# Optimization experiments

Hardware: AMD Instinct MI355X
Metric: run time of the kernel (lower is better)

Reference implementation:

```python
import jax, jax.numpy as jnp
import numpy as np

I = 256  # input size
H = 256  # hidden size
B = 128
S = 1024
EPS = 1e-5


def setup_inputs() -> dict:
    key = jax.random.key(0)
    ks = jax.random.split(key, 8)
    bound = 1.0 / np.sqrt(H)
    x = jax.random.normal(ks[0], (B, S, I), dtype=jnp.float32)
    mask = jax.random.randint(ks[1], (B, S), 0, 2) == 1
    W_ih = jax.random.uniform(ks[2], (4 * H, I), jnp.float32, -bound, bound)
    W_hh = jax.random.uniform(ks[3], (4 * H, H), jnp.float32, -bound, bound)
    b_ih = jax.random.uniform(ks[4], (4 * H,), jnp.float32, -bound, bound)
    b_hh = jax.random.uniform(ks[5], (4 * H,), jnp.float32, -bound, bound)
    gamma = jnp.ones((H,), jnp.float32)
    beta = jnp.zeros((H,), jnp.float32)
    return {"x": x, "mask": mask, "W_ih": W_ih, "W_hh": W_hh,
            "b_ih": b_ih, "b_hh": b_hh, "gamma": gamma, "beta": beta}


def _layernorm(h, gamma, beta):
    mu = jnp.mean(h, axis=-1, keepdims=True)
    var = jnp.var(h, axis=-1, keepdims=True)
    return (h - mu) * jax.lax.rsqrt(var + EPS) * gamma + beta


def reference(x, mask, W_ih, W_hh, b_ih, b_hh, gamma, beta):
    b = x.shape[0]
    h0 = jnp.zeros((b, H), x.dtype)
    c0 = jnp.zeros((b, H), x.dtype)
    out0 = jnp.zeros((b, H), x.dtype)

    def step(carry, inp):
        h, c, out = carry
        x_t, m_t = inp  # (B,I), (B,)
        hn = _layernorm(h, gamma, beta)
        gates = x_t @ W_ih.T + b_ih + hn @ W_hh.T + b_hh  # (B,4H)
        i_g, f_g, g_g, o_g = jnp.split(gates, 4, axis=-1)
        c = jax.nn.sigmoid(f_g) * c + jax.nn.sigmoid(i_g) * jnp.tanh(g_g)
        h = jax.nn.sigmoid(o_g) * jnp.tanh(c)
        # output[~mask] = h[~mask]; where mask is True the old output is kept
        out = jnp.where(m_t[:, None], out, h)
        return (h, c, out), None

    xs = (jnp.swapaxes(x, 0, 1), jnp.swapaxes(mask, 0, 1))  # (S,B,I), (S,B)
    (h, c, out), _ = jax.lax.scan(step, (h0, c0, out0), xs)
    return out
```

## Files before the change

kernel.cpp:

```cpp
#include <hip/hip_runtime.h>
#include <hip/hip_bf16.h>
#include <stdint.h>


#define Bb 128
#define Ss 1024
#define Ii 256
#define Hh 256
#define G4v 1024
#define EPSF 1e-5f

typedef __bf16 bf16;
typedef __attribute__((ext_vector_type(8))) __bf16 bf16x8;
typedef __attribute__((ext_vector_type(4))) __bf16 bf16x4;
typedef __attribute__((ext_vector_type(4))) float f32x4;
typedef unsigned int u32;
typedef unsigned long long u64;

static __device__ __forceinline__ f32x4 mfma16(bf16x8 a, bf16x8 b, f32x4 c) {
  return __builtin_amdgcn_mfma_f32_16x16x32_bf16(a, b, c, 0, 0, 0);
}
static __device__ __forceinline__ float sigm(float x) { return 1.0f / (1.0f + __expf(-x)); }
static __device__ __forceinline__ float tanhf_(float x) {
  float e = __expf(-2.0f * fabsf(x));
  float t = (1.0f - e) / (1.0f + e);
  return x < 0.0f ? -t : t;
}
static __device__ __forceinline__ bf16 bfu(unsigned short u) {
  return __builtin_bit_cast(bf16, u);
}
static __device__ __forceinline__ unsigned short ubf(bf16 b) {
  return __builtin_bit_cast(unsigned short, b);
}

__global__ void k_conv_wih(const float* __restrict__ W, bf16* __restrict__ hi,
                           bf16* __restrict__ lo) {
  int i = (blockIdx.x * 256 + threadIdx.x) * 4;
  f32x4 v = *(const f32x4*)(W + i);
  bf16x4 h_, l_;
#pragma unroll
  for (int j = 0; j < 4; ++j) {
    bf16 hh = (bf16)v[j];
    h_[j] = hh;
    l_[j] = (bf16)(v[j] - (float)hh);
  }
  *(bf16x4*)(hi + i) = h_;
  *(bf16x4*)(lo + i) = l_;
}

__global__ void k_prep_whh(const float* __restrict__ W, const float* __restrict__ gamma,
                           bf16* __restrict__ Whi, bf16* __restrict__ Wlo) {
  int tid = blockIdx.x * 256 + threadIdx.x;
  int lane = tid & 63;
  int fk = tid >> 6;
  int ntg = fk >> 3, kt = fk & 7;
  int g = ntg * 16 + (lane & 15);
  int k = kt * 32 + ((lane >> 4) << 3);
  bf16x8 rh, rl;
#pragma unroll
  for (int j = 0; j < 8; ++j) {
    float wv = W[g * Hh + k + j] * gamma[k + j];
    bf16 hh = (bf16)wv;
    rh[j] = hh;
    rl[j] = (bf16)(wv - (float)hh);
  }
  *(bf16x8*)(Whi + (size_t)tid * 8) = rh;
  *(bf16x8*)(Wlo + (size_t)tid * 8) = rl;
}

__global__ void k_prep_rd(const float* __restrict__ W, const float* __restrict__ gamma,
                          const float* __restrict__ beta, const float* __restrict__ bih,
                          const float* __restrict__ bhh, float* __restrict__ RD) {
  int g = blockIdx.x * 256 + threadIdx.x;
  float r = 0.f, d = 0.f;
  for (int k = 0; k < Hh; ++k) {
    float w = W[g * Hh + k];
    r += w * gamma[k];
    d += w * beta[k];
  }
  RD[2 * g] = r;
  RD[2 * g + 1] = d + bih[g] + bhh[g];
}

__global__ __launch_bounds__(256, 2) void k_gemm(const float* __restrict__ x,
                                                 const bf16* __restrict__ Whi,
                                                 const bf16* __restrict__ Wlo,
                                                 float* __restrict__ xw,
                                                 int t0, int Tc, int ntb) {
  __shared__ bf16 Bs[2][128 * 128];
  int bid = blockIdx.x;
  int b = bid & 127;
  int r2 = bid >> 7;
  int tb = r2 % ntb;
  int gt = r2 / ntb;
  int g0 = gt * 128;
  int tid = threadIdx.x, w = tid >> 6, lane = tid & 63;
  int li = lane & 15, lg = lane >> 4;
  char* BsB = (char*)Bs;
  int tbase = tb * 128 + 32 * w;
  f32x4 acc[2][8];
#pragma unroll
  for (int mt = 0; mt < 2; ++mt)
#pragma unroll
    for (int nt = 0; nt < 8; ++nt) acc[mt][nt] = (f32x4){0.f, 0.f, 0.f, 0.f};

  for (int kp = 0; kp < 2; ++kp) {
#pragma unroll
    for (int it = 0; it < 8; ++it) {
      int p = it * 4096 + tid * 16;
      int row = p >> 8, colb = p & 255;
      size_t goff = (size_t)(g0 + row) * 512 + kp * 256 + colb;
      int dst = row * 256 + (colb ^ ((row & 7) << 4));
      *(bf16x8*)(BsB + dst) = *(const bf16x8*)((const char*)Whi + goff);
      *(bf16x8*)(BsB + 32768 + dst) = *(const bf16x8*)((const char*)Wlo + goff);
    }
    __syncthreads();
#pragma unroll
    for (int kt = 0; kt < 4; ++kt) {
      int kl = kt * 32 + lg * 8;
      int kgl = kp * 128 + kl;
      bf16x8 ah[2], al[2];
#pragma unroll
      for (int mt = 0; mt < 2; ++mt) {
        int t = t0 + tbase + 16 * mt + li;
        const float* xp = x + ((size_t)b * Ss + t) * Ii + kgl;
        f32x4 f0 = *(const f32x4*)xp;
        f32x4 f1 = *(const f32x4*)(xp + 4);
        bf16x8 hv, lv;
#pragma unroll
        for (int j = 0; j < 4; ++j) {
          bf16 h0 = (bf16)f0[j];
          hv[j] = h0;
          lv[j] = (bf16)(f0[j] - (float)h0);
          bf16 h1 = (bf16)f1[j];
          hv[4 + j] = h1;
          lv[4 + j] = (bf16)(f1[j] - (float)h1);
        }
        ah[mt] = hv;
        al[mt] = lv;
      }
#pragma unroll
      for (int nt = 0; nt < 8; ++nt) {
        int grow = nt * 16 + li;
        int off = grow * 256 + ((kl * 2) ^ ((grow & 7) << 4));
        bf16x8 bh = *(const bf16x8*)(BsB + off);
        bf16x8 bl = *(const bf16x8*)(BsB + 32768 + off);
#pragma unroll
        for (int mt = 0; mt < 2; ++mt) {
          acc[mt][nt] = mfma16(ah[mt], bh, acc[mt][nt]);
          acc[mt][nt] = mfma16(ah[mt], bl, acc[mt][nt]);
          acc[mt][nt] = mfma16(al[mt], bh, acc[mt][nt]);
        }
      }
    }
    __syncthreads();
  }
#pragma unroll
  for (int mt = 0; mt < 2; ++mt)
#pragma unroll
    for (int nt = 0; nt < 8; ++nt)
#pragma unroll
      for (int r = 0; r < 4; ++r) {
        int tl = tbase + 16 * mt + lg * 4 + r;
        int g = g0 + nt * 16 + li;
        xw[((size_t)b * Tc + tl) * G4v + g] = acc[mt][nt][r];
      }
}

__global__ __launch_bounds__(256, 1) void k_recur(
    const bf16* __restrict__ Whi_f, const bf16* __restrict__ Wlo_f,
    const float* __restrict__ xw, const int* __restrict__ mask,
    const float* __restrict__ RD, float* __restrict__ st_h, float* __restrict__ st_c,
    float* __restrict__ st_o, u64* pub, float* __restrict__ out,
    int t0, int Tc, int first, int last) {
  __shared__ bf16 hb[2][16 * 256];
  __shared__ float murs[2][16][2];
  __shared__ float2 spw[4][16];
  __shared__ float spart[16][16][2];
  int bid = blockIdx.x;
  int grp = bid & 7, q = bid >> 3;
  int tid = threadIdx.x, w = tid >> 6, lane = tid & 63;
  int li = lane & 15, lg = lane >> 4;
  int b0 = grp * 16;
  int jloc = (q * 4 + w) * 16 + li;
  char* hbB = (char*)hb;

  bf16x8 wph[4][8], wpl[4][8];
#pragma unroll
  for (int c = 0; c < 4; ++c)
#pragma unroll
    for (int kt = 0; kt < 8; ++kt) {
      int ntg = c * 16 + q * 4 + w;
      size_t off = ((size_t)(ntg * 8 + kt) * 64 + lane) * 8;
      wph[c][kt] = *(const bf16x8*)(Whi_f + off);
      wpl[c][kt] = *(const bf16x8*)(Wlo_f + off);
      asm volatile("" : "+a"(wph[c][kt]), "+a"(wpl[c][kt]));
    }
  float Rr[4], Dd[4];
#pragma unroll
  for (int c = 0; c < 4; ++c) {
    int g = c * 256 + jloc;
    Rr[c] = RD[2 * g];
    Dd[c] = RD[2 * g + 1];
  }

  float cst[4], ost[4];
  if (first) {
#pragma unroll
    for (int i = 0; i < 16; ++i) {
      hb[0][tid * 16 + i] = (bf16)0.0f;
      hb[1][tid * 16 + i] = (bf16)0.0f;
    }
#pragma unroll
    for (int r = 0; r < 4; ++r) { cst[r] = 0.f; ost[r] = 0.f; }
    if (tid < 16) { murs[0][tid][0] = 0.f; murs[0][tid][1] = rsqrtf(EPSF); }
  } else {
    int row = tid >> 4, cs = tid & 15, jseg = cs * 16;
    float s = 0.f, ss = 0.f;
#pragma unroll
    for (int i = 0; i < 16; ++i) {
      float v = st_h[(size_t)(b0 + row) * Hh + jseg + i];
      s += v;
      ss += v * v;
      bf16 hh = (bf16)v;
      int boff = row * 512 + (((jseg + i) * 2) ^ ((row & 7) << 4));
      *(bf16*)(hbB + boff) = hh;
      *(bf16*)(hbB + 8192 + boff) = (bf16)(v - (float)hh);
    }
    spart[row][cs][0] = s;
    spart[row][cs][1] = ss;
#pragma unroll
    for (int r = 0; r < 4; ++r) {
      int m = lg * 4 + r;
      cst[r] = st_c[(size_t)(b0 + m) * Hh + jloc];
      ost[r] = st_o[(size_t)(b0 + m) * Hh + jloc];
    }
    __syncthreads();
    if (tid < 16) {
      float s2 = 0.f, ss2 = 0.f;
#pragma unroll
      for (int i = 0; i < 16; ++i) { s2 += spart[tid][i][0]; ss2 += spart[tid][i][1]; }
      float mu = s2 * (1.f / 256.f);
      float var = ss2 * (1.f / 256.f) - mu * mu;
      float rs = rsqrtf(var + EPSF);
      murs[0][tid][0] = mu * rs;
      murs[0][tid][1] = rs;
    }
  }
  __syncthreads();

  float xwv[4][4];
  int mk[4];
#pragma unroll
  for (int c = 0; c < 4; ++c)
#pragma unroll
    for (int r = 0; r < 4; ++r)
      xwv[c][r] = xw[((size_t)(b0 + lg * 4 + r) * Tc + 0) * G4v + c * 256 + jloc];
#pragma unroll
  for (int r = 0; r < 4; ++r) mk[r] = mask[(size_t)(b0 + lg * 4 + r) * Ss + t0];

  int grow = tid >> 4, gcg = tid & 15;

  for (int tl = 0; tl < Tc; ++tl) {
    int tg = t0 + tl;
    int slot = (tg + 1) & 1;
    u32 want = (u32)(tg + 1);

    f32x4 acc[4];
#pragma unroll
    for (int c = 0; c < 4; ++c) acc[c] = (f32x4){0.f, 0.f, 0.f, 0.f};
#pragma unroll
    for (int kt = 0; kt < 8; ++kt) {
      int aoff = li * 512 + (((kt * 32 + lg * 8) * 2) ^ ((li & 7) << 4));
      bf16x8 ah = *(const bf16x8*)(hbB + aoff);
      bf16x8 al = *(const bf16x8*)(hbB + 8192 + aoff);
#pragma unroll
      for (int c = 0; c < 4; ++c) {
        acc[c] = mfma16(ah, wph[c][kt], acc[c]);
        acc[c] = mfma16(ah, wpl[c][kt], acc[c]);
        acc[c] = mfma16(al, wph[c][kt], acc[c]);
      }
    }
    float mrs[4], rsv[4];
#pragma unroll
    for (int r = 0; r < 4; ++r) {
      int m = lg * 4 + r;
      mrs[r] = murs[tl & 1][m][0];
      rsv[r] = murs[tl & 1][m][1];
    }
    __syncthreads();

    float hnew[4];
#pragma unroll
    for (int r = 0; r < 4; ++r) {
      float i_ = acc[0][r] * rsv[r] - mrs[r] * Rr[0] + Dd[0] + xwv[0][r];
      float f_ = acc[1][r] * rsv[r] - mrs[r] * Rr[1] + Dd[1] + xwv[1][r];
      float g_ = acc[2][r] * rsv[r] - mrs[r] * Rr[2] + Dd[2] + xwv[2][r];
      float o_ = acc[3][r] * rsv[r] - mrs[r] * Rr[3] + Dd[3] + xwv[3][r];
      float cn = sigm(f_) * cst[r] + sigm(i_) * tanhf_(g_);
      float hn = sigm(o_) * tanhf_(cn);
      cst[r] = cn;
      ost[r] = mk[r] ? ost[r] : hn;
      hnew[r] = hn;
    }
    u64* ph = pub + (size_t)(slot * 32 + bid) * 1024;
#pragma unroll
    for (int r = 0; r < 4; ++r) {
      int m = lg * 4 + r;
      float hn = hnew[r];
      bf16 hh = (bf16)hn;
      bf16 hl = (bf16)(hn - (float)hh);
      int boff = m * 512 + ((jloc * 2) ^ ((m & 7) << 4));
      *(bf16*)(hbB + boff) = hh;
      *(bf16*)(hbB + 8192 + boff) = hl;
      u64 pv = ((u64)want << 32) | ((u32)ubf(hh) << 16) | (u32)ubf(hl);
      __hip_atomic_store(&ph[m * 64 + (w * 16 + li)], pv, __ATOMIC_RELAXED,
                         __HIP_MEMORY_SCOPE_AGENT);
    }
    {
      float sr[4], qr[4];
#pragma unroll
      for (int r = 0; r < 4; ++r) { sr[r] = hnew[r]; qr[r] = hnew[r] * hnew[r]; }
#pragma unroll
      for (int msk = 1; msk < 16; msk <<= 1)
#pragma unroll
        for (int r = 0; r < 4; ++r) {
          sr[r] += __shfl_xor(sr[r], msk);
          qr[r] += __shfl_xor(qr[r], msk);
        }
      if (li == 0)
#pragma unroll
        for (int r = 0; r < 4; ++r) spw[w][lg * 4 + r] = make_float2(sr[r], qr[r]);
    }
    if (tl == Tc - 1) {
#pragma unroll
      for (int r = 0; r < 4; ++r) {
        int m = lg * 4 + r;
        st_h[(size_t)(b0 + m) * Hh + jloc] = hnew[r];
        st_c[(size_t)(b0 + m) * Hh + jloc] = cst[r];
        st_o[(size_t)(b0 + m) * Hh + jloc] = ost[r];
      }
      if (last) {
#pragma unroll
        for (int r = 0; r < 4; ++r) out[(size_t)(b0 + lg * 4 + r) * Hh + jloc] = ost[r];
      }
    }
    {
      int tln = (tl + 1 < Tc) ? tl + 1 : Tc - 1;
#pragma unroll
      for (int c = 0; c < 4; ++c)
#pragma unroll
        for (int r = 0; r < 4; ++r)
          xwv[c][r] = xw[((size_t)(b0 + lg * 4 + r) * Tc + tln) * G4v + c * 256 + jloc];
#pragma unroll
      for (int r = 0; r < 4; ++r) mk[r] = mask[(size_t)(b0 + lg * 4 + r) * Ss + t0 + tln];
    }

    u64 gv[3][4];
    const u64* srcs[3];
#pragma unroll
    for (int pi = 0; pi < 3; ++pi) {
      int qq = (q + 1 + pi) & 3;
      int pbid = qq * 8 + grp;
      srcs[pi] = pub + (size_t)(slot * 32 + pbid) * 1024 + grow * 64 + gcg * 4;
#pragma unroll
      for (int e = 0; e < 4; ++e)
        gv[pi][e] = __hip_atomic_load(&srcs[pi][e], __ATOMIC_RELAXED,
                                      __HIP_MEMORY_SCOPE_AGENT);
    }
    {
      int cnt = 0;
      bool ok = false;
      while (!ok) {
        ok = true;
#pragma unroll
        for (int pi = 0; pi < 3; ++pi)
#pragma unroll
          for (int e = 0; e < 4; ++e)
            if ((u32)(gv[pi][e] >> 32) != want) {
              ok = false;
              gv[pi][e] = __hip_atomic_load(&srcs[pi][e], __ATOMIC_RELAXED,
                                            __HIP_MEMORY_SCOPE_AGENT);
            }
        if (++cnt > (1 << 22)) break;
      }
    }
    float su = 0.f, qu = 0.f;
#pragma unroll
    for (int pi = 0; pi < 3; ++pi) {
      int qq = (q + 1 + pi) & 3;
      int j0 = qq * 64 + gcg * 4;
      int boff = grow * 512 + ((j0 * 2) ^ ((grow & 7) << 4));
      bf16x4 h4, l4;
#pragma unroll
      for (int e = 0; e < 4; ++e) {
        u32 d = (u32)gv[pi][e];
        bf16 hh = bfu((unsigned short)(d >> 16));
        bf16 hl = bfu((unsigned short)(d & 0xffffu));
        h4[e] = hh;
        l4[e] = hl;
        float f = (float)hh + (float)hl;
        su += f;
        qu += f * f;
      }
      *(bf16x4*)(hbB + boff) = h4;
      *(bf16x4*)(hbB + 8192 + boff) = l4;
    }
#pragma unroll
    for (int msk = 1; msk < 16; msk <<= 1) {
      su += __shfl_xor(su, msk);
      qu += __shfl_xor(qu, msk);
    }
    __syncthreads();
    if (li == 0) {
      float s = su + spw[0][grow].x + spw[1][grow].x + spw[2][grow].x + spw[3][grow].x;
      float ss2 = qu + spw[0][grow].y + spw[1][grow].y + spw[2][grow].y + spw[3][grow].y;
      float mu = s * (1.f / 256.f);
      float var = ss2 * (1.f / 256.f) - mu * mu;
      float rs = rsqrtf(var + EPSF);
      murs[(tl + 1) & 1][grow][0] = mu * rs;
      murs[(tl + 1) & 1][grow][1] = rs;
    }
  }
}

extern "C" void kernel_launch(void* const* d_in, const int* in_sizes, int n_in,
                              void* d_out, int out_size, void* d_ws, size_t ws_size,
                              hipStream_t stream) {
  (void)in_sizes; (void)n_in; (void)out_size;
  const float* x = (const float*)d_in[0];
  const int* mask = (const int*)d_in[1];
  const float* Wih = (const float*)d_in[2];
  const float* Whh = (const float*)d_in[3];
  const float* bih = (const float*)d_in[4];
  const float* bhh = (const float*)d_in[5];
  const float* gamma = (const float*)d_in[6];
  const float* beta = (const float*)d_in[7];
  float* outp = (float*)d_out;
  char* ws = (char*)d_ws;

  const size_t extra = 4 * (512u << 10) + (8u << 10) + 3 * (128u << 10) +
                       (512u << 10) + (64u << 10);
  int Tc = 128;
  if (ws_size >= (size_t)1024 * 524288 + extra) Tc = 1024;
  else if (ws_size >= (size_t)512 * 524288 + extra) Tc = 512;
  else if (ws_size >= (size_t)256 * 524288 + extra) Tc = 256;

  size_t o = 0;
  auto take = [&](size_t bytes) { size_t r = o; o += (bytes + 255) & ~(size_t)255; return r; };
  size_t xw_off = take((size_t)Bb * Tc * G4v * 4);
  size_t wihh_off = take(512u << 10);
  size_t wihl_off = take(512u << 10);
  size_t whhh_off = take(512u << 10);
  size_t whhl_off = take(512u << 10);
  size_t rd_off = take(8u << 10);
  size_t sth_off = take(128u << 10);
  size_t stc_off = take(128u << 10);
  size_t sto_off = take(128u << 10);
  size_t pub_off = take(512u << 10);

  bf16* wihh = (bf16*)(ws + wihh_off);
  bf16* wihl = (bf16*)(ws + wihl_off);
  bf16* whhh = (bf16*)(ws + whhh_off);
  bf16* whhl = (bf16*)(ws + whhl_off);
  float* rd = (float*)(ws + rd_off);
  float* xwp = (float*)(ws + xw_off);
  float* sth = (float*)(ws + sth_off);
  float* stc = (float*)(ws + stc_off);
  float* sto = (float*)(ws + sto_off);
  u64* pubh = (u64*)(ws + pub_off);

  hipMemsetAsync(pubh, 0, 512u << 10, stream);
  k_conv_wih<<<dim3(256), dim3(256), 0, stream>>>(Wih, wihh, wihl);
  k_prep_whh<<<dim3(128), dim3(256), 0, stream>>>(Whh, gamma, whhh, whhl);
  k_prep_rd<<<dim3(4), dim3(256), 0, stream>>>(Whh, gamma, beta, bih, bhh, rd);

  int nchunk = Ss / Tc;
  int ntb = Tc / 128;
  for (int ci = 0; ci < nchunk; ++ci) {
    int t0 = ci * Tc;
    k_gemm<<<dim3(8 * ntb * 128), dim3(256), 0, stream>>>(x, wihh, wihl, xwp, t0, Tc, ntb);
    k_recur<<<dim3(32), dim3(256), 0, stream>>>(whhh, whhl, xwp, mask, rd, sth, stc, sto,
                                                pubh, outp, t0, Tc,
                                                ci == 0 ? 1 : 0, ci == nchunk - 1 ? 1 : 0);
  }
}
```

Measured before the change: 4.769 ms.

## Switch recurrent GEMM to fp16 split-hidden with single fp16 weight, hoist peer loads

The recurrent step now stores W_hh as a single fp16 matrix instead of bf16 hi/lo pairs. It keeps h as an fp16 hi/lo split, so each step issues 2 MFMAs per tile instead of 3, into two independent accumulators. It also issues the atomic loads of peer blocks' published hidden values earlier, before the state/output bookkeeping, so their latency overlaps that work, and it simplifies the spin-wait check. This cuts MFMA count and register pressure on the serial critical path. The cost is lower weight precision (fp16 without a lo term) and possible fp16 range issues.

```diff
diff --git a/kernel.cpp b/kernel.cpp
--- a/kernel.cpp
+++ b/kernel.cpp
@@ -11,14 +11,20 @@
 #define EPSF 1e-5f
 
 typedef __bf16 bf16;
+typedef _Float16 f16;
 typedef __attribute__((ext_vector_type(8))) __bf16 bf16x8;
 typedef __attribute__((ext_vector_type(4))) __bf16 bf16x4;
+typedef __attribute__((ext_vector_type(8))) _Float16 f16x8;
+typedef __attribute__((ext_vector_type(4))) _Float16 f16x4;
 typedef __attribute__((ext_vector_type(4))) float f32x4;
 typedef unsigned int u32;
 typedef unsigned long long u64;
 
-static __device__ __forceinline__ f32x4 mfma16(bf16x8 a, bf16x8 b, f32x4 c) {
+static __device__ __forceinline__ f32x4 mfma16b(bf16x8 a, bf16x8 b, f32x4 c) {
   return __builtin_amdgcn_mfma_f32_16x16x32_bf16(a, b, c, 0, 0, 0);
+}
+static __device__ __forceinline__ f32x4 mfma16h(f16x8 a, f16x8 b, f32x4 c) {
+  return __builtin_amdgcn_mfma_f32_16x16x32_f16(a, b, c, 0, 0, 0);
 }
 static __device__ __forceinline__ float sigm(float x) { return 1.0f / (1.0f + __expf(-x)); }
 static __device__ __forceinline__ float tanhf_(float x) {
@@ -26,11 +32,11 @@
   float t = (1.0f - e) / (1.0f + e);
   return x < 0.0f ? -t : t;
 }
-static __device__ __forceinline__ bf16 bfu(unsigned short u) {
-  return __builtin_bit_cast(bf16, u);
-}
-static __device__ __forceinline__ unsigned short ubf(bf16 b) {
-  return __builtin_bit_cast(unsigned short, b);
+static __device__ __forceinline__ unsigned short ush(f16 h) {
+  return __builtin_bit_cast(unsigned short, h);
+}
+static __device__ __forceinline__ f16 hus(unsigned short u) {
+  return __builtin_bit_cast(f16, u);
 }
 
 __global__ void k_conv_wih(const float* __restrict__ W, bf16* __restrict__ hi,
@@ -49,23 +55,17 @@
 }
 
 __global__ void k_prep_whh(const float* __restrict__ W, const float* __restrict__ gamma,
-                           bf16* __restrict__ Whi, bf16* __restrict__ Wlo) {
+                           f16* __restrict__ Wf) {
   int tid = blockIdx.x * 256 + threadIdx.x;
   int lane = tid & 63;
   int fk = tid >> 6;
   int ntg = fk >> 3, kt = fk & 7;
   int g = ntg * 16 + (lane & 15);
   int k = kt * 32 + ((lane >> 4) << 3);
-  bf16x8 rh, rl;
-#pragma unroll
-  for (int j = 0; j < 8; ++j) {
-    float wv = W[g * Hh + k + j] * gamma[k + j];
-    bf16 hh = (bf16)wv;
-    rh[j] = hh;
-    rl[j] = (bf16)(wv - (float)hh);
-  }
-  *(bf16x8*)(Whi + (size_t)tid * 8) = rh;
-  *(bf16x8*)(Wlo + (size_t)tid * 8) = rl;
+  f16x8 r;
+#pragma unroll
+  for (int j = 0; j < 8; ++j) r[j] = (f16)(W[g * Hh + k + j] * gamma[k + j]);
+  *(f16x8*)(Wf + (size_t)tid * 8) = r;
 }
 
 __global__ void k_prep_rd(const float* __restrict__ W, const float* __restrict__ gamma,
@@ -147,9 +147,9 @@
         bf16x8 bl = *(const bf16x8*)(BsB + 32768 + off);
 #pragma unroll
         for (int mt = 0; mt < 2; ++mt) {
-          acc[mt][nt] = mfma16(ah[mt], bh, acc[mt][nt]);
-          acc[mt][nt] = mfma16(ah[mt], bl, acc[mt][nt]);
-          acc[mt][nt] = mfma16(al[mt], bh, acc[mt][nt]);
+          acc[mt][nt] = mfma16b(ah[mt], bh, acc[mt][nt]);
+          acc[mt][nt] = mfma16b(ah[mt], bl, acc[mt][nt]);
+          acc[mt][nt] = mfma16b(al[mt], bh, acc[mt][nt]);
         }
       }
     }
@@ -168,12 +168,11 @@
 }
 
 __global__ __launch_bounds__(256, 1) void k_recur(
-    const bf16* __restrict__ Whi_f, const bf16* __restrict__ Wlo_f,
-    const float* __restrict__ xw, const int* __restrict__ mask,
-    const float* __restrict__ RD, float* __restrict__ st_h, float* __restrict__ st_c,
-    float* __restrict__ st_o, u64* pub, float* __restrict__ out,
-    int t0, int Tc, int first, int last) {
-  __shared__ bf16 hb[2][16 * 256];
+    const f16* __restrict__ Wf, const float* __restrict__ xw,
+    const int* __restrict__ mask, const float* __restrict__ RD,
+    float* __restrict__ st_h, float* __restrict__ st_c, float* __restrict__ st_o,
+    u64* pub, float* __restrict__ out, int t0, int Tc, int first, int last) {
+  __shared__ f16 hb[2][16 * 256];
   __shared__ float murs[2][16][2];
   __shared__ float2 spw[4][16];
   __shared__ float spart[16][16][2];
@@ -185,16 +184,14 @@
   int jloc = (q * 4 + w) * 16 + li;
   char* hbB = (char*)hb;
 
-  bf16x8 wph[4][8], wpl[4][8];
+  f16x8 wp[4][8];
 #pragma unroll
   for (int c = 0; c < 4; ++c)
 #pragma unroll
     for (int kt = 0; kt < 8; ++kt) {
       int ntg = c * 16 + q * 4 + w;
-      size_t off = ((size_t)(ntg * 8 + kt) * 64 + lane) * 8;
-      wph[c][kt] = *(const bf16x8*)(Whi_f + off);
-      wpl[c][kt] = *(const bf16x8*)(Wlo_f + off);
-      asm volatile("" : "+a"(wph[c][kt]), "+a"(wpl[c][kt]));
+      wp[c][kt] = *(const f16x8*)(Wf + ((size_t)(ntg * 8 + kt) * 64 + lane) * 8);
+      asm volatile("" : "+a"(wp[c][kt]));
     }
   float Rr[4], Dd[4];
 #pragma unroll
@@ -208,8 +205,8 @@
   if (first) {
 #pragma unroll
     for (int i = 0; i < 16; ++i) {
-      hb[0][tid * 16 + i] = (bf16)0.0f;
-      hb[1][tid * 16 + i] = (bf16)0.0f;
+      hb[0][tid * 16 + i] = (f16)0.0f;
+      hb[1][tid * 16 + i] = (f16)0.0f;
     }
 #pragma unroll
     for (int r = 0; r < 4; ++r) { cst[r] = 0.f; ost[r] = 0.f; }
@@ -222,10 +219,10 @@
       float v = st_h[(size_t)(b0 + row) * Hh + jseg + i];
       s += v;
       ss += v * v;
-      bf16 hh = (bf16)v;
+      f16 hh = (f16)v;
       int boff = row * 512 + (((jseg + i) * 2) ^ ((row & 7) << 4));
-      *(bf16*)(hbB + boff) = hh;
-      *(bf16*)(hbB + 8192 + boff) = (bf16)(v - (float)hh);
+      *(f16*)(hbB + boff) = hh;
+      *(f16*)(hbB + 8192 + boff) = (f16)(v - (float)hh);
     }
     spart[row][cs][0] = s;
     spart[row][cs][1] = ss;
@@ -266,19 +263,21 @@
     int slot = (tg + 1) & 1;
     u32 want = (u32)(tg + 1);
 
-    f32x4 acc[4];
-#pragma unroll
-    for (int c = 0; c < 4; ++c) acc[c] = (f32x4){0.f, 0.f, 0.f, 0.f};
+    f32x4 a0[4], a1[4];
+#pragma unroll
+    for (int c = 0; c < 4; ++c) {
+      a0[c] = (f32x4){0.f, 0.f, 0.f, 0.f};
+      a1[c] = (f32x4){0.f, 0.f, 0.f, 0.f};
+    }
 #pragma unroll
     for (int kt = 0; kt < 8; ++kt) {
       int aoff = li * 512 + (((kt * 32 + lg * 8) * 2) ^ ((li & 7) << 4));
-      bf16x8 ah = *(const bf16x8*)(hbB + aoff);
-      bf16x8 al = *(const bf16x8*)(hbB + 8192 + aoff);
+      f16x8 ah = *(const f16x8*)(hbB + aoff);
+      f16x8 al = *(const f16x8*)(hbB + 8192 + aoff);
 #pragma unroll
       for (int c = 0; c < 4; ++c) {
-        acc[c] = mfma16(ah, wph[c][kt], acc[c]);
-        acc[c] = mfma16(ah, wpl[c][kt], acc[c]);
-        acc[c] = mfma16(al, wph[c][kt], acc[c]);
+        a0[c] = mfma16h(ah, wp[c][kt], a0[c]);
+        a1[c] = mfma16h(al, wp[c][kt], a1[c]);
       }
     }
     float mrs[4], rsv[4];
@@ -293,10 +292,10 @@
     float hnew[4];
 #pragma unroll
     for (int r = 0; r < 4; ++r) {
-      float i_ = acc[0][r] * rsv[r] - mrs[r] * Rr[0] + Dd[0] + xwv[0][r];
-      float f_ = acc[1][r] * rsv[r] - mrs[r] * Rr[1] + Dd[1] + xwv[1][r];
-      float g_ = acc[2][r] * rsv[r] - mrs[r] * Rr[2] + Dd[2] + xwv[2][r];
-      float o_ = acc[3][r] * rsv[r] - mrs[r] * Rr[3] + Dd[3] + xwv[3][r];
+      float i_ = (a0[0][r] + a1[0][r]) * rsv[r] - mrs[r] * Rr[0] + Dd[0] + xwv[0][r];
+      float f_ = (a0[1][r] + a1[1][r]) * rsv[r] - mrs[r] * Rr[1] + Dd[1] + xwv[1][r];
+      float g_ = (a0[2][r] + a1[2][r]) * rsv[r] - mrs[r] * Rr[2] + Dd[2] + xwv[2][r];
+      float o_ = (a0[3][r] + a1[3][r]) * rsv[r] - mrs[r] * Rr[3] + Dd[3] + xwv[3][r];
       float cn = sigm(f_) * cst[r] + sigm(i_) * tanhf_(g_);
       float hn = sigm(o_) * tanhf_(cn);
       cst[r] = cn;
@@ -308,15 +307,29 @@
     for (int r = 0; r < 4; ++r) {
       int m = lg * 4 + r;
       float hn = hnew[r];
-      bf16 hh = (bf16)hn;
-      bf16 hl = (bf16)(hn - (float)hh);
+      f16 hh = (f16)hn;
+      f16 hl = (f16)(hn - (float)hh);
       int boff = m * 512 + ((jloc * 2) ^ ((m & 7) << 4));
-      *(bf16*)(hbB + boff) = hh;
-      *(bf16*)(hbB + 8192 + boff) = hl;
-      u64 pv = ((u64)want << 32) | ((u32)ubf(hh) << 16) | (u32)ubf(hl);
+      *(f16*)(hbB + boff) = hh;
+      *(f16*)(hbB + 8192 + boff) = hl;
+      u64 pv = ((u64)want << 32) | ((u32)ush(hh) << 16) | (u32)ush(hl);
       __hip_atomic_store(&ph[m * 64 + (w * 16 + li)], pv, __ATOMIC_RELAXED,
                          __HIP_MEMORY_SCOPE_AGENT);
     }
+
+    u64 gv[3][4];
+    const u64* srcs[3];
+#pragma unroll
+    for (int pi = 0; pi < 3; ++pi) {
+      int qq = (q + 1 + pi) & 3;
+      int pbid = qq * 8 + grp;
+      srcs[pi] = pub + (size_t)(slot * 32 + pbid) * 1024 + grow * 64 + gcg * 4;
+#pragma unroll
+      for (int e = 0; e < 4; ++e)
+        gv[pi][e] = __hip_atomic_load(&srcs[pi][e], __ATOMIC_RELAXED,
+                                      __HIP_MEMORY_SCOPE_AGENT);
+    }
+
     {
       float sr[4], qr[4];
 #pragma unroll
@@ -356,33 +369,26 @@
       for (int r = 0; r < 4; ++r) mk[r] = mask[(size_t)(b0 + lg * 4 + r) * Ss + t0 + tln];
     }
 
-    u64 gv[3][4];
-    const u64* srcs[3];
-#pragma unroll
-    for (int pi = 0; pi < 3; ++pi) {
-      int qq = (q + 1 + pi) & 3;
-      int pbid = qq * 8 + grp;
-      srcs[pi] = pub + (size_t)(slot * 32 + pbid) * 1024 + grow * 64 + gcg * 4;
-#pragma unroll
-      for (int e = 0; e < 4; ++e)
-        gv[pi][e] = __hip_atomic_load(&srcs[pi][e], __ATOMIC_RELAXED,
-                                      __HIP_MEMORY_SCOPE_AGENT);
-    }
     {
+      u32 bad = 0;
+#pragma unroll
+      for (int pi = 0; pi < 3; ++pi)
+#pragma unroll
+        for (int e = 0; e < 4; ++e) bad |= (u32)(gv[pi][e] >> 32) ^ want;
       int cnt = 0;
-      bool ok = false;
-      while (!ok) {
-        ok = true;
+      while (bad) {
 #pragma unroll
         for (int pi = 0; pi < 3; ++pi)
 #pragma unroll
           for (int e = 0; e < 4; ++e)
-            if ((u32)(gv[pi][e] >> 32) != want) {
-              ok = false;
-              gv[pi][e] = __hip_atomic_load(&srcs[pi][e], __ATOMIC_RELAXED,
-                                            __HIP_MEMORY_SCOPE_AGENT);
-            }
-        if (++cnt > (1 << 22)) break;
+            gv[pi][e] = __hip_atomic_load(&srcs[pi][e], __ATOMIC_RELAXED,
+                                          __HIP_MEMORY_SCOPE_AGENT);
+        bad = 0;
+#pragma unroll
+        for (int pi = 0; pi < 3; ++pi)
+#pragma unroll
+          for (int e = 0; e < 4; ++e) bad |= (u32)(gv[pi][e] >> 32) ^ want;
+        if (++cnt > (1 << 20)) break;
       }
     }
     float su = 0.f, qu = 0.f;
@@ -391,20 +397,20 @@
       int qq = (q + 1 + pi) & 3;
       int j0 = qq * 64 + gcg * 4;
       int boff = grow * 512 + ((j0 * 2) ^ ((grow & 7) << 4));
-      bf16x4 h4, l4;
+      f16x4 h4, l4;
 #pragma unroll
       for (int e = 0; e < 4; ++e) {
         u32 d = (u32)gv[pi][e];
-        bf16 hh = bfu((unsigned short)(d >> 16));
-        bf16 hl = bfu((unsigned short)(d & 0xffffu));
+        f16 hh = hus((unsigned short)(d >> 16));
+        f16 hl = hus((unsigned short)(d & 0xffffu));
         h4[e] = hh;
         l4[e] = hl;
         float f = (float)hh + (float)hl;
         su += f;
         qu += f * f;
       }
-      *(bf16x4*)(hbB + boff) = h4;
-      *(bf16x4*)(hbB + 8192 + boff) = l4;
+      *(f16x4*)(hbB + boff) = h4;
+      *(f16x4*)(hbB + 8192 + boff) = l4;
     }
 #pragma unroll
     for (int msk = 1; msk < 16; msk <<= 1) {
@@ -439,7 +445,7 @@
   float* outp = (float*)d_out;
   char* ws = (char*)d_ws;
 
-  const size_t extra = 4 * (512u << 10) + (8u << 10) + 3 * (128u << 10) +
+  const size_t extra = 3 * (512u << 10) + (8u << 10) + 3 * (128u << 10) +
                        (512u << 10) + (64u << 10);
   int Tc = 128;
   if (ws_size >= (size_t)1024 * 524288 + extra) Tc = 1024;
@@ -451,8 +457,7 @@
   size_t xw_off = take((size_t)Bb * Tc * G4v * 4);
   size_t wihh_off = take(512u << 10);
   size_t wihl_off = take(512u << 10);
-  size_t whhh_off = take(512u << 10);
-  size_t whhl_off = take(512u << 10);
+  size_t whh_off = take(512u << 10);
   size_t rd_off = take(8u << 10);
   size_t sth_off = take(128u << 10);
   size_t stc_off = take(128u << 10);
@@ -461,8 +466,7 @@
 
   bf16* wihh = (bf16*)(ws + wihh_off);
   bf16* wihl = (bf16*)(ws + wihl_off);
-  bf16* whhh = (bf16*)(ws + whhh_off);
-  bf16* whhl = (bf16*)(ws + whhl_off);
+  f16* whhf = (f16*)(ws + whh_off);
   float* rd = (float*)(ws + rd_off);
   float* xwp = (float*)(ws + xw_off);
   float* sth = (float*)(ws + sth_off);
@@ -472,7 +476,7 @@
 
   hipMemsetAsync(pubh, 0, 512u << 10, stream);
   k_conv_wih<<<dim3(256), dim3(256), 0, stream>>>(Wih, wihh, wihl);
-  k_prep_whh<<<dim3(128), dim3(256), 0, stream>>>(Whh, gamma, whhh, whhl);
+  k_prep_whh<<<dim3(128), dim3(256), 0, stream>>>(Whh, gamma, whhf);
   k_prep_rd<<<dim3(4), dim3(256), 0, stream>>>(Whh, gamma, beta, bih, bhh, rd);
 
   int nchunk = Ss / Tc;
@@ -480,7 +484,7 @@
   for (int ci = 0; ci < nchunk; ++ci) {
     int t0 = ci * Tc;
     k_gemm<<<dim3(8 * ntb * 128), dim3(256), 0, stream>>>(x, wihh, wihl, xwp, t0, Tc, ntb);
-    k_recur<<<dim3(32), dim3(256), 0, stream>>>(whhh, whhl, xwp, mask, rd, sth, stc, sto,
+    k_recur<<<dim3(32), dim3(256), 0, stream>>>(whhf, xwp, mask, rd, sth, stc, sto,
                                                 pubh, outp, t0, Tc,
                                                 ci == 0 ? 1 : 0, ci == nchunk - 1 ? 1 : 0);
   }
```

Result: no change. 4.757 ms (-0.3%).
